# Performance work log

Hardware: AMD Instinct MI355X
Metric: run time of the kernel (lower is better)

Reference implementation:

```python
import jax, jax.numpy as jnp
import numpy as np

NUM_HEADS = 8
D_MODEL = 512
D_K = D_MODEL // NUM_HEADS


def setup_inputs() -> dict:
    key = jax.random.key(0)
    ks = jax.random.split(key, 8)
    B, C, L = 4, D_MODEL, 2048
    s = 1.0 / np.sqrt(C)  # xavier-ish scale for 1x1 convs
    return {
        "X_q": jax.random.normal(ks[0], (B, C, L), jnp.float32),
        "X_k": jax.random.normal(ks[1], (B, C, L), jnp.float32),
        "X_v": jax.random.normal(ks[2], (B, C, L), jnp.float32),
        "Wq": jax.random.normal(ks[3], (D_MODEL, C), jnp.float32) * s,
        "Wk": jax.random.normal(ks[4], (D_MODEL, C), jnp.float32) * s,
        "Wv": jax.random.normal(ks[5], (D_MODEL, C), jnp.float32) * s,
        "Wh": jax.random.normal(ks[6], (D_MODEL, D_MODEL), jnp.float32) * s,
        "bh": jnp.zeros((D_MODEL,), jnp.float32),
    }


def reference(X_q, X_k, X_v, Wq, Wk, Wv, Wh, bh):
    B, C, L = X_q.shape
    H, dk = NUM_HEADS, D_K

    def proj(x, W):  # 1x1 Conv1d, no bias: (B,Cin,L) -> (B,Cout,L)
        return jnp.einsum("oc,bcl->bol", W, x)

    # split_heads: (B, d_model, L) -> (B, H, d_k, L)
    Q = proj(X_q, Wq).reshape(B, H, dk, L)
    K = proj(X_k, Wk).reshape(B, H, dk, L)
    V = proj(X_v, Wv).reshape(B, H, dk, L)

    Q = Q / np.sqrt(dk).astype(np.float32)
    # scores: Q^T K -> (B, H, L_q, L_k)
    scores = jnp.einsum("bhdq,bhdk->bhqk", Q, K)
    A = jax.nn.softmax(scores, axis=-1)
    # H = A @ V^T -> (B, H, L, d_k); dropout is identity at eval
    Hh = jnp.einsum("bhqk,bhdk->bhqd", A, V)
    # group_heads: (B,H,L,dk) -> (B,H,dk,L) -> (B, d_model, L)
    H_cat = Hh.transpose(0, 1, 3, 2).reshape(B, H * dk, L)
    out = jnp.einsum("oc,bcl->bol", Wh, H_cat) + bh[None, :, None]
    return (out, A)
```

## Files before the change

kernel.cpp:

```cpp
#include <hip/hip_runtime.h>

#define L_SEQ 2048
#define CDIM  512
#define NB    4
#define NH    8
#define DKH   64

typedef __attribute__((ext_vector_type(8))) __bf16 bf16x8;
typedef __attribute__((ext_vector_type(4))) float  f32x4;
typedef __attribute__((ext_vector_type(8))) unsigned short u16x8;

__device__ __forceinline__ unsigned short f2bf(float f) {
  union { float f; unsigned u; } x; x.f = f;
  unsigned r = x.u + 0x7FFFu + ((x.u >> 16) & 1u);
  return (unsigned short)(r >> 16);
}
__device__ __forceinline__ float bf2f(unsigned short u) {
  union { unsigned u; float f; } x; x.u = ((unsigned)u) << 16;
  return x.f;
}
__device__ __forceinline__ bf16x8 ldfrag(const unsigned short* p) {
  u16x8 v = *reinterpret_cast<const u16x8*>(p);
  return __builtin_bit_cast(bf16x8, v);
}
__device__ __forceinline__ bf16x8 asbf(u16x8 v) { return __builtin_bit_cast(bf16x8, v); }
__device__ __forceinline__ float fexp2(float x) {
  float r; asm("v_exp_f32 %0, %1" : "=v"(r) : "v"(x)); return r;
}
#define MFMA(a,b,c) __builtin_amdgcn_mfma_f32_16x16x32_bf16((a),(b),(c),0,0,0)

__device__ __forceinline__ void loadset(u16x8* dst, const unsigned short* base,
                                        int kt, long stride) {
#pragma unroll
  for (int t = 0; t < 4; ++t) {
    const unsigned short* p = base + (size_t)(kt + t * 16) * stride;
    dst[2*t]   = *reinterpret_cast<const u16x8*>(p);
    dst[2*t+1] = *reinterpret_cast<const u16x8*>(p + 32);
  }
}

__global__ __launch_bounds__(256) void k_cast(const float* __restrict__ X,
                                              unsigned short* __restrict__ Y, int n) {
  int i = (blockIdx.x * 256 + threadIdx.x) * 8;
  if (i + 8 > n) return;
  const float4* p = reinterpret_cast<const float4*>(X + i);
  float4 a = p[0], b = p[1];
  u16x8 o;
  o[0]=f2bf(a.x); o[1]=f2bf(a.y); o[2]=f2bf(a.z); o[3]=f2bf(a.w);
  o[4]=f2bf(b.x); o[5]=f2bf(b.y); o[6]=f2bf(b.z); o[7]=f2bf(b.w);
  *reinterpret_cast<u16x8*>(Y + i) = o;
}

__global__ __launch_bounds__(256) void k_transpose(const float* __restrict__ X,
                                                   unsigned short* __restrict__ Xt) {
  __shared__ __align__(16) unsigned short t[64][72];
  int l0 = blockIdx.x * 64, c0 = blockIdx.y * 64;
  size_t boff = (size_t)blockIdx.z * CDIM * L_SEQ;
  const float* Xb = X + boff;
  unsigned short* Xtb = Xt + boff;
  int tid = threadIdx.x;
  int cc = tid >> 2, lo = (tid & 3) * 16;
  const float* src = Xb + (size_t)(c0 + cc) * L_SEQ + l0 + lo;
#pragma unroll
  for (int i = 0; i < 4; ++i) {
    float4 v = *reinterpret_cast<const float4*>(src + i * 4);
    t[lo + i*4 + 0][cc] = f2bf(v.x);
    t[lo + i*4 + 1][cc] = f2bf(v.y);
    t[lo + i*4 + 2][cc] = f2bf(v.z);
    t[lo + i*4 + 3][cc] = f2bf(v.w);
  }
  __syncthreads();
  int ll = tid >> 2, co = (tid & 3) * 16;
  unsigned short* dst = Xtb + (size_t)(l0 + ll) * CDIM + c0 + co;
  u16x8 a = *reinterpret_cast<const u16x8*>(&t[ll][co]);
  u16x8 b = *reinterpret_cast<const u16x8*>(&t[ll][co + 8]);
  *reinterpret_cast<u16x8*>(dst) = a;
  *reinterpret_cast<u16x8*>(dst + 8) = b;
}

template<int OUT_BF16, int HAS_BIAS>
__global__ __launch_bounds__(256) void k_gemm_nt(
    const unsigned short* __restrict__ A, long sA,
    const unsigned short* __restrict__ Bt, long sB,
    void* __restrict__ Out, long sO,
    const float* __restrict__ bias, float scale, int M, int N) {
  __shared__ __align__(16) unsigned short lA[128 * 64];
  __shared__ __align__(16) unsigned short lB[128 * 64];
  int b = blockIdx.z;
  const unsigned short* Ab = A + (size_t)b * sA;
  const unsigned short* Bb = Bt + (size_t)b * sB;
  int m0 = blockIdx.y * 128, n0 = blockIdx.x * 128;
  int tid = threadIdx.x, lane = tid & 63, wave = tid >> 6;
  int wm = (wave >> 1) * 64, wn = (wave & 1) * 64;
  f32x4 acc[4][4] = {};
  int srow = tid >> 3;
  int sslot = tid & 7;

  for (int k0 = 0; k0 < 512; k0 += 64) {
    __syncthreads();
#pragma unroll
    for (int i = 0; i < 4; ++i) {
      int r = srow + 32 * i;
      int sw = (sslot ^ (r & 7)) * 8;
      u16x8 va = *reinterpret_cast<const u16x8*>(Ab + (size_t)(m0 + r) * 512 + k0 + sslot * 8);
      *reinterpret_cast<u16x8*>(&lA[r * 64 + sw]) = va;
      u16x8 vb = *reinterpret_cast<const u16x8*>(Bb + (size_t)(n0 + r) * 512 + k0 + sslot * 8);
      *reinterpret_cast<u16x8*>(&lB[r * 64 + sw]) = vb;
    }
    __syncthreads();
#pragma unroll
    for (int c = 0; c < 2; ++c) {
      bf16x8 af[4], bfr[4];
#pragma unroll
      for (int t = 0; t < 4; ++t) {
        int ra = wm + t * 16 + (lane & 15);
        int sa = (lane >> 4) + 4 * c;
        af[t] = ldfrag(&lA[ra * 64 + ((sa ^ (ra & 7)) * 8)]);
        int rb = wn + t * 16 + (lane & 15);
        bfr[t] = ldfrag(&lB[rb * 64 + ((sa ^ (rb & 7)) * 8)]);
      }
#pragma unroll
      for (int i = 0; i < 4; ++i)
#pragma unroll
        for (int j = 0; j < 4; ++j)
          acc[i][j] = MFMA(af[i], bfr[j], acc[i][j]);
    }
  }
  int row4 = (lane >> 4) * 4, col = lane & 15;
#pragma unroll
  for (int i = 0; i < 4; ++i)
#pragma unroll
    for (int j = 0; j < 4; ++j)
#pragma unroll
      for (int e = 0; e < 4; ++e) {
        int r = m0 + wm + i * 16 + row4 + e;
        int cN = n0 + wn + j * 16 + col;
        float v = acc[i][j][e] * scale;
        if (HAS_BIAS) v += bias[r];
        size_t idx = (size_t)b * sO + (size_t)r * N + cN;
        if (OUT_BF16) ((unsigned short*)Out)[idx] = f2bf(v);
        else          ((float*)Out)[idx] = v;
      }
}

__global__ __launch_bounds__(256) void k_attn(
    const unsigned short* __restrict__ Qt,
    const unsigned short* __restrict__ Kt,
    const unsigned short* __restrict__ Vn,
    unsigned short* __restrict__ HhT,
    float* __restrict__ Aout) {
  __shared__ __align__(16) unsigned short al[4][1024];
  int bh = blockIdx.y;
  int b = bh >> 3, h = bh & 7;
  int lane = threadIdx.x & 63, wave = threadIdx.x >> 6;
  int q0 = blockIdx.x * 64 + wave * 16;
  const unsigned short* Qh = Qt + (size_t)b * L_SEQ * CDIM + h * DKH;
  const unsigned short* Kh = Kt + (size_t)b * L_SEQ * CDIM + h * DKH;
  const unsigned short* Vh = Vn + (size_t)b * CDIM * L_SEQ + (size_t)h * DKH * L_SEQ;
  unsigned short* Ho = HhT + (size_t)b * L_SEQ * CDIM + h * DKH;
  float* Ab = Aout + (size_t)bh * L_SEQ * L_SEQ;

  int fr = lane & 15, fg = lane >> 4;
  bf16x8 qf0 = ldfrag(Qh + (size_t)(q0 + fr) * CDIM + fg * 8);
  bf16x8 qf1 = ldfrag(Qh + (size_t)(q0 + fr) * CDIM + fg * 8 + 32);

  const unsigned short* kbase = Kh + (size_t)fr * CDIM + fg * 8;
  const unsigned short* vbase = Vh + (size_t)fr * L_SEQ + fg * 8;

  float psum[4] = {0.f, 0.f, 0.f, 0.f};
  {
    u16x8 ka[8], kb2[8];
    auto half1 = [&](const u16x8* ks) {
#pragma unroll
      for (int t = 0; t < 4; ++t) {
        f32x4 s = {0.f, 0.f, 0.f, 0.f};
        s = MFMA(qf0, asbf(ks[2*t]), s);
        s = MFMA(qf1, asbf(ks[2*t+1]), s);
#pragma unroll
        for (int e = 0; e < 4; ++e) psum[e] += fexp2(s[e]);
      }
    };
    loadset(ka, kbase, 0, CDIM);
    for (int i = 0; i < 32; i += 2) {
      loadset(kb2, kbase, (i + 1) * 64, CDIM);
      half1(ka);
      loadset(ka, kbase, ((i + 2) & 31) * 64, CDIM);
      half1(kb2);
    }
  }
#pragma unroll
  for (int e = 0; e < 4; ++e) {
    psum[e] += __shfl_xor(psum[e], 1, 64);
    psum[e] += __shfl_xor(psum[e], 2, 64);
    psum[e] += __shfl_xor(psum[e], 4, 64);
    psum[e] += __shfl_xor(psum[e], 8, 64);
  }
  float inv[4];
#pragma unroll
  for (int e = 0; e < 4; ++e) inv[e] = 1.0f / psum[e];

  f32x4 oacc[4] = {};
  unsigned short* alw = al[wave];
  {
    u16x8 ka[8], kb2[8];
    auto half2 = [&](const u16x8* ks, int kt) {
      u16x8 vr[8];
      loadset(vr, vbase, 0, 0);
#pragma unroll
      for (int nt = 0; nt < 4; ++nt) {
        const unsigned short* vp = vbase + (size_t)(nt * 16) * L_SEQ + kt;
        vr[2*nt]   = *reinterpret_cast<const u16x8*>(vp);
        vr[2*nt+1] = *reinterpret_cast<const u16x8*>(vp + 32);
      }
#pragma unroll
      for (int t = 0; t < 4; ++t) {
        f32x4 s = {0.f, 0.f, 0.f, 0.f};
        s = MFMA(qf0, asbf(ks[2*t]), s);
        s = MFMA(qf1, asbf(ks[2*t+1]), s);
#pragma unroll
        for (int e = 0; e < 4; ++e) {
          float a = fexp2(s[e]) * inv[e];
          int row = fg * 4 + e;
          int byte = (row * 128 + (t * 16 + fr) * 2) ^ ((row & 7) << 4);
          alw[byte >> 1] = f2bf(a);
        }
      }
      {
        int wrow = lane >> 2;
        int slot0 = (lane & 3) * 2;
        int by0 = (wrow * 128 + slot0 * 16) ^ ((wrow & 7) << 4);
        int by1 = (wrow * 128 + (slot0 + 1) * 16) ^ ((wrow & 7) << 4);
        u16x8 p0 = *reinterpret_cast<const u16x8*>(alw + (by0 >> 1));
        u16x8 p1 = *reinterpret_cast<const u16x8*>(alw + (by1 >> 1));
        float* dp = Ab + (size_t)(q0 + wrow) * L_SEQ + kt + (lane & 3) * 16;
        f32x4 f0 = {bf2f(p0[0]), bf2f(p0[1]), bf2f(p0[2]), bf2f(p0[3])};
        f32x4 f1 = {bf2f(p0[4]), bf2f(p0[5]), bf2f(p0[6]), bf2f(p0[7])};
        f32x4 f2 = {bf2f(p1[0]), bf2f(p1[1]), bf2f(p1[2]), bf2f(p1[3])};
        f32x4 f3 = {bf2f(p1[4]), bf2f(p1[5]), bf2f(p1[6]), bf2f(p1[7])};
        *reinterpret_cast<f32x4*>(dp + 0)  = f0;
        *reinterpret_cast<f32x4*>(dp + 4)  = f1;
        *reinterpret_cast<f32x4*>(dp + 8)  = f2;
        *reinterpret_cast<f32x4*>(dp + 12) = f3;
      }
      int byA0 = (fr * 128 + fg * 16) ^ ((fr & 7) << 4);
      int byA1 = (fr * 128 + (fg + 4) * 16) ^ ((fr & 7) << 4);
      bf16x8 af0 = ldfrag(alw + (byA0 >> 1));
      bf16x8 af1 = ldfrag(alw + (byA1 >> 1));
#pragma unroll
      for (int nt = 0; nt < 4; ++nt) {
        oacc[nt] = MFMA(af0, asbf(vr[2*nt]), oacc[nt]);
        oacc[nt] = MFMA(af1, asbf(vr[2*nt+1]), oacc[nt]);
      }
    };
    loadset(ka, kbase, 0, CDIM);
    for (int i = 0; i < 32; i += 2) {
      loadset(kb2, kbase, (i + 1) * 64, CDIM);
      half2(ka, i * 64);
      loadset(ka, kbase, ((i + 2) & 31) * 64, CDIM);
      half2(kb2, (i + 1) * 64);
    }
  }
#pragma unroll
  for (int nt = 0; nt < 4; ++nt)
#pragma unroll
    for (int e = 0; e < 4; ++e)
      Ho[(size_t)(q0 + fg * 4 + e) * CDIM + nt * 16 + fr] = f2bf(oacc[nt][e]);
}

extern "C" void kernel_launch(void* const* d_in, const int* in_sizes, int n_in,
                              void* d_out, int out_size, void* d_ws, size_t ws_size,
                              hipStream_t stream) {
  const float* Xq = (const float*)d_in[0];
  const float* Xk = (const float*)d_in[1];
  const float* Xv = (const float*)d_in[2];
  const float* Wq = (const float*)d_in[3];
  const float* Wk = (const float*)d_in[4];
  const float* Wv = (const float*)d_in[5];
  const float* Wh = (const float*)d_in[6];
  const float* bh = (const float*)d_in[7];

  const size_t PROJ = (size_t)NB * L_SEQ * CDIM;
  float* out_f = (float*)d_out;
  float* A_out = out_f + PROJ;

  unsigned short* Qt = (unsigned short*)d_out;
  unsigned short* Kt = Qt + PROJ;
  unsigned short* Xtq = (unsigned short*)A_out;
  unsigned short* Xtk = Xtq + PROJ;
  unsigned short* Xtv = Xtk + PROJ;
  unsigned short* Vn  = (unsigned short*)d_ws;
  unsigned short* HhT = Vn + PROJ;
  unsigned short* Wqb = HhT + PROJ;
  unsigned short* Wkb = Wqb + CDIM * CDIM;
  unsigned short* Wvb = Wkb + CDIM * CDIM;
  unsigned short* Whb = Wvb + CDIM * CDIM;

  int nW = CDIM * CDIM;
  k_cast<<<nW / 2048, 256, 0, stream>>>(Wq, Wqb, nW);
  k_cast<<<nW / 2048, 256, 0, stream>>>(Wk, Wkb, nW);
  k_cast<<<nW / 2048, 256, 0, stream>>>(Wv, Wvb, nW);
  k_cast<<<nW / 2048, 256, 0, stream>>>(Wh, Whb, nW);

  dim3 tg(L_SEQ / 64, CDIM / 64, NB);
  k_transpose<<<tg, 256, 0, stream>>>(Xq, Xtq);
  k_transpose<<<tg, 256, 0, stream>>>(Xk, Xtk);
  k_transpose<<<tg, 256, 0, stream>>>(Xv, Xtv);

  const long sLC = (long)L_SEQ * CDIM;
  k_gemm_nt<1, 0><<<dim3(CDIM / 128, L_SEQ / 128, NB), 256, 0, stream>>>(
      Xtq, sLC, Wqb, 0, Qt, sLC, nullptr, 0.18033688f, L_SEQ, CDIM);
  k_gemm_nt<1, 0><<<dim3(CDIM / 128, L_SEQ / 128, NB), 256, 0, stream>>>(
      Xtk, sLC, Wkb, 0, Kt, sLC, nullptr, 1.0f, L_SEQ, CDIM);
  k_gemm_nt<1, 0><<<dim3(L_SEQ / 128, CDIM / 128, NB), 256, 0, stream>>>(
      Wvb, 0, Xtv, sLC, Vn, sLC, nullptr, 1.0f, CDIM, L_SEQ);

  k_attn<<<dim3(L_SEQ / 64, NB * NH), 256, 0, stream>>>(Qt, Kt, Vn, HhT, A_out);

  k_gemm_nt<0, 1><<<dim3(L_SEQ / 128, CDIM / 128, NB), 256, 0, stream>>>(
      Whb, 0, HhT, sLC, out_f, sLC, bh, 1.0f, CDIM, L_SEQ);
}
```

Before: 519.8 us.

## Transpose score MFMA to keep P in registers and drop LDS staging

Swaps the MFMA operand order so each lane holds four consecutive key scores of one query row. The probabilities can then be written straight to A as float4 stores and packed into bf16 A-operand fragments in registers, with no LDS round trip. V loads are split into 4-element pieces so their k ordering matches the new P fragment layout. This removes the shared-memory buffer, its writes and reads, and the bf16-to-float re-expansion, and it shrinks the row-sum reduction to two shuffles. The A stores become strided per lane, 16 bytes per row, which may coalesce less well than before.

After: 571.9 us. 10.0% more time.

```diff
diff --git a/kernel.cpp b/kernel.cpp
--- a/kernel.cpp
+++ b/kernel.cpp
@@ -9,15 +9,13 @@
 typedef __attribute__((ext_vector_type(8))) __bf16 bf16x8;
 typedef __attribute__((ext_vector_type(4))) float  f32x4;
 typedef __attribute__((ext_vector_type(8))) unsigned short u16x8;
+typedef __attribute__((ext_vector_type(4))) unsigned short u16x4;
+typedef __attribute__((ext_vector_type(4))) unsigned int  u32x4;
 
 __device__ __forceinline__ unsigned short f2bf(float f) {
   union { float f; unsigned u; } x; x.f = f;
   unsigned r = x.u + 0x7FFFu + ((x.u >> 16) & 1u);
   return (unsigned short)(r >> 16);
-}
-__device__ __forceinline__ float bf2f(unsigned short u) {
-  union { unsigned u; float f; } x; x.u = ((unsigned)u) << 16;
-  return x.f;
 }
 __device__ __forceinline__ bf16x8 ldfrag(const unsigned short* p) {
   u16x8 v = *reinterpret_cast<const u16x8*>(p);
@@ -149,7 +147,6 @@
     const unsigned short* __restrict__ Vn,
     unsigned short* __restrict__ HhT,
     float* __restrict__ Aout) {
-  __shared__ __align__(16) unsigned short al[4][1024];
   int bh = blockIdx.y;
   int b = bh >> 3, h = bh & 7;
   int lane = threadIdx.x & 63, wave = threadIdx.x >> 6;
@@ -165,19 +162,18 @@
   bf16x8 qf1 = ldfrag(Qh + (size_t)(q0 + fr) * CDIM + fg * 8 + 32);
 
   const unsigned short* kbase = Kh + (size_t)fr * CDIM + fg * 8;
-  const unsigned short* vbase = Vh + (size_t)fr * L_SEQ + fg * 8;
-
-  float psum[4] = {0.f, 0.f, 0.f, 0.f};
+  const unsigned short* vbase = Vh + (size_t)fr * L_SEQ + fg * 4;
+
+  float psum = 0.f;
   {
     u16x8 ka[8], kb2[8];
     auto half1 = [&](const u16x8* ks) {
 #pragma unroll
       for (int t = 0; t < 4; ++t) {
         f32x4 s = {0.f, 0.f, 0.f, 0.f};
-        s = MFMA(qf0, asbf(ks[2*t]), s);
-        s = MFMA(qf1, asbf(ks[2*t+1]), s);
-#pragma unroll
-        for (int e = 0; e < 4; ++e) psum[e] += fexp2(s[e]);
+        s = MFMA(asbf(ks[2*t]), qf0, s);
+        s = MFMA(asbf(ks[2*t+1]), qf1, s);
+        psum += fexp2(s[0]) + fexp2(s[1]) + fexp2(s[2]) + fexp2(s[3]);
       }
     };
     loadset(ka, kbase, 0, CDIM);
@@ -188,68 +184,48 @@
       half1(kb2);
     }
   }
-#pragma unroll
-  for (int e = 0; e < 4; ++e) {
-    psum[e] += __shfl_xor(psum[e], 1, 64);
-    psum[e] += __shfl_xor(psum[e], 2, 64);
-    psum[e] += __shfl_xor(psum[e], 4, 64);
-    psum[e] += __shfl_xor(psum[e], 8, 64);
-  }
-  float inv[4];
-#pragma unroll
-  for (int e = 0; e < 4; ++e) inv[e] = 1.0f / psum[e];
+  psum += __shfl_xor(psum, 16, 64);
+  psum += __shfl_xor(psum, 32, 64);
+  float inv = 1.0f / psum;
 
   f32x4 oacc[4] = {};
-  unsigned short* alw = al[wave];
   {
     u16x8 ka[8], kb2[8];
     auto half2 = [&](const u16x8* ks, int kt) {
-      u16x8 vr[8];
-      loadset(vr, vbase, 0, 0);
+      u16x4 v0a[4], v0b[4], v1a[4], v1b[4];
 #pragma unroll
       for (int nt = 0; nt < 4; ++nt) {
         const unsigned short* vp = vbase + (size_t)(nt * 16) * L_SEQ + kt;
-        vr[2*nt]   = *reinterpret_cast<const u16x8*>(vp);
-        vr[2*nt+1] = *reinterpret_cast<const u16x8*>(vp + 32);
-      }
+        v0a[nt] = *reinterpret_cast<const u16x4*>(vp);
+        v0b[nt] = *reinterpret_cast<const u16x4*>(vp + 16);
+        v1a[nt] = *reinterpret_cast<const u16x4*>(vp + 32);
+        v1b[nt] = *reinterpret_cast<const u16x4*>(vp + 48);
+      }
+      unsigned int w[4][2];
 #pragma unroll
       for (int t = 0; t < 4; ++t) {
         f32x4 s = {0.f, 0.f, 0.f, 0.f};
-        s = MFMA(qf0, asbf(ks[2*t]), s);
-        s = MFMA(qf1, asbf(ks[2*t+1]), s);
-#pragma unroll
-        for (int e = 0; e < 4; ++e) {
-          float a = fexp2(s[e]) * inv[e];
-          int row = fg * 4 + e;
-          int byte = (row * 128 + (t * 16 + fr) * 2) ^ ((row & 7) << 4);
-          alw[byte >> 1] = f2bf(a);
-        }
-      }
-      {
-        int wrow = lane >> 2;
-        int slot0 = (lane & 3) * 2;
-        int by0 = (wrow * 128 + slot0 * 16) ^ ((wrow & 7) << 4);
-        int by1 = (wrow * 128 + (slot0 + 1) * 16) ^ ((wrow & 7) << 4);
-        u16x8 p0 = *reinterpret_cast<const u16x8*>(alw + (by0 >> 1));
-        u16x8 p1 = *reinterpret_cast<const u16x8*>(alw + (by1 >> 1));
-        float* dp = Ab + (size_t)(q0 + wrow) * L_SEQ + kt + (lane & 3) * 16;
-        f32x4 f0 = {bf2f(p0[0]), bf2f(p0[1]), bf2f(p0[2]), bf2f(p0[3])};
-        f32x4 f1 = {bf2f(p0[4]), bf2f(p0[5]), bf2f(p0[6]), bf2f(p0[7])};
-        f32x4 f2 = {bf2f(p1[0]), bf2f(p1[1]), bf2f(p1[2]), bf2f(p1[3])};
-        f32x4 f3 = {bf2f(p1[4]), bf2f(p1[5]), bf2f(p1[6]), bf2f(p1[7])};
-        *reinterpret_cast<f32x4*>(dp + 0)  = f0;
-        *reinterpret_cast<f32x4*>(dp + 4)  = f1;
-        *reinterpret_cast<f32x4*>(dp + 8)  = f2;
-        *reinterpret_cast<f32x4*>(dp + 12) = f3;
-      }
-      int byA0 = (fr * 128 + fg * 16) ^ ((fr & 7) << 4);
-      int byA1 = (fr * 128 + (fg + 4) * 16) ^ ((fr & 7) << 4);
-      bf16x8 af0 = ldfrag(alw + (byA0 >> 1));
-      bf16x8 af1 = ldfrag(alw + (byA1 >> 1));
+        s = MFMA(asbf(ks[2*t]), qf0, s);
+        s = MFMA(asbf(ks[2*t+1]), qf1, s);
+        float a0 = fexp2(s[0]) * inv;
+        float a1 = fexp2(s[1]) * inv;
+        float a2 = fexp2(s[2]) * inv;
+        float a3 = fexp2(s[3]) * inv;
+        f32x4 av = {a0, a1, a2, a3};
+        *reinterpret_cast<f32x4*>(Ab + (size_t)(q0 + fr) * L_SEQ + kt + t * 16 + fg * 4) = av;
+        w[t][0] = ((unsigned int)f2bf(a1) << 16) | f2bf(a0);
+        w[t][1] = ((unsigned int)f2bf(a3) << 16) | f2bf(a2);
+      }
+      u32x4 p0w = {w[0][0], w[0][1], w[1][0], w[1][1]};
+      u32x4 p1w = {w[2][0], w[2][1], w[3][0], w[3][1]};
+      bf16x8 pa0 = __builtin_bit_cast(bf16x8, p0w);
+      bf16x8 pa1 = __builtin_bit_cast(bf16x8, p1w);
 #pragma unroll
       for (int nt = 0; nt < 4; ++nt) {
-        oacc[nt] = MFMA(af0, asbf(vr[2*nt]), oacc[nt]);
-        oacc[nt] = MFMA(af1, asbf(vr[2*nt+1]), oacc[nt]);
+        u16x8 vv0 = __builtin_shufflevector(v0a[nt], v0b[nt], 0, 1, 2, 3, 4, 5, 6, 7);
+        u16x8 vv1 = __builtin_shufflevector(v1a[nt], v1b[nt], 0, 1, 2, 3, 4, 5, 6, 7);
+        oacc[nt] = MFMA(pa0, asbf(vv0), oacc[nt]);
+        oacc[nt] = MFMA(pa1, asbf(vv1), oacc[nt]);
       }
     };
     loadset(ka, kbase, 0, CDIM);
```
